# Optimization experiments

Hardware: AMD Instinct MI355X
Metric: run time of the kernel (lower is better)

## Reference

```python
import jax, jax.numpy as jnp
import numpy as np

N_NODES = 100000
N_EDGES = 3200000
N_GRAPHS = 128
F_IN, HID = 16, 64


def setup_inputs() -> dict:
    key = jax.random.key(0)
    ks = jax.random.split(key, 16)
    def lin(k, fan_in, fan_out):
        bound = 1.0 / np.sqrt(fan_in)
        kw, kb = jax.random.split(k)
        W = jax.random.uniform(kw, (fan_in, fan_out), jnp.float32, -bound, bound)
        b = jax.random.uniform(kb, (fan_out,), jnp.float32, -bound, bound)
        return W, b
    x = jax.random.normal(ks[0], (N_NODES, F_IN), jnp.float32)
    edge_index = jax.random.randint(ks[1], (2, N_EDGES), 0, N_NODES, jnp.int64 if jax.config.jax_enable_x64 else jnp.int32)
    edge_attr = jax.random.normal(ks[2], (N_EDGES, 4), jnp.float32)
    batch = jnp.sort(jax.random.randint(ks[3], (N_NODES,), 0, N_GRAPHS))
    W1, b1 = lin(ks[4], F_IN, HID)
    W2, b2 = lin(ks[5], HID, HID)
    W3, b3 = lin(ks[6], HID, HID)
    Wf1, bf1 = lin(ks[7], HID, 32)
    Wf2, bf2 = lin(ks[8], 32, 1)
    return dict(x=x, edge_index=edge_index, edge_attr=edge_attr, batch=batch,
                W1=W1, b1=b1, W2=W2, b2=b2, W3=W3, b3=b3,
                Wf1=Wf1, bf1=bf1, Wf2=Wf2, bf2=bf2)


def _gcn_conv(x, src, dst, norm, W, b, n_nodes):
    # PyG GCNConv: out = scatter_add(norm * (x @ W)[src] -> dst) + b
    h = x @ W                                   # [N, out]
    msg = h[src] * norm[:, None]                # [E+N, out] gather + scale
    agg = jax.ops.segment_sum(msg, dst, num_segments=n_nodes)
    return agg + b


def reference(x, edge_index, edge_attr, batch, W1, b1, W2, b2, W3, b3, Wf1, bf1, Wf2, bf2):
    n = x.shape[0]
    # add self loops (GCNConv default)
    loop = jnp.arange(n, dtype=edge_index.dtype)
    src = jnp.concatenate([edge_index[0], loop])
    dst = jnp.concatenate([edge_index[1], loop])
    # symmetric degree normalization: deg computed on dst with self loops
    deg = jax.ops.segment_sum(jnp.ones_like(src, dtype=x.dtype), dst, num_segments=n)
    dinv = jax.lax.rsqrt(jnp.maximum(deg, 1.0))
    norm = dinv[src] * dinv[dst]

    h = jax.nn.relu(_gcn_conv(x, src, dst, norm, W1, b1, n))   # dropout = identity (eval)
    h = jax.nn.relu(_gcn_conv(h, src, dst, norm, W2, b2, n))
    h = jax.nn.relu(_gcn_conv(h, src, dst, norm, W3, b3, n))

    # global mean pool over graphs
    sums = jax.ops.segment_sum(h, batch, num_segments=N_GRAPHS)          # [B, HID]
    cnts = jax.ops.segment_sum(jnp.ones((n,), x.dtype), batch, num_segments=N_GRAPHS)
    pooled = sums / jnp.maximum(cnts, 1.0)[:, None]

    z = jax.nn.relu(pooled @ Wf1 + bf1)
    return z @ Wf2 + bf2                                                  # [B, 1]
```

## Files before the change

### kernel.cpp

```cpp
#include <hip/hip_runtime.h>
#include <hip/hip_bf16.h>

#define HID 64
#define MAXNB 2048
#define NBLK 128
#define FILL_T 1024
#define SENT 0xFFFFFFFFu

__device__ __forceinline__ float bf2f(unsigned short u) {
    return __uint_as_float(((unsigned)u) << 16);
}
__device__ __forceinline__ unsigned short f2bf(float f) {
    __hip_bfloat16 b = __float2bfloat16(f);
    return *(unsigned short*)&b;
}
__device__ __host__ __forceinline__ int ceil16(int c) { return (c + 15) & ~15; }


__global__ __launch_bounds__(FILL_T) void radix_hist_kernel(
    const int* __restrict__ ei, int* __restrict__ H, int* __restrict__ bhist,
    int* __restrict__ bhist_pad, int E, int NB, int C) {
    __shared__ int lh[MAXNB];
    int blk = blockIdx.x, tid = threadIdx.x;
    for (int i = tid; i < NB; i += FILL_T) lh[i] = 0;
    __syncthreads();
    int lo = blk * C, hi = min(lo + C, E);
    for (int e = lo + tid; e < hi; e += FILL_T) atomicAdd(&lh[ei[E + e] >> 6], 1);
    __syncthreads();
    for (int i = tid; i < NB; i += FILL_T) {
        int v = lh[i];
        H[blk * NB + i] = v;
        if (v) {
            atomicAdd(&bhist[i], v);
            atomicAdd(&bhist_pad[i], ceil16(v));
        }
    }
}

__global__ __launch_bounds__(256) void scan_kernel(
    const int* __restrict__ bhist, const int* __restrict__ bhist_pad,
    int* __restrict__ pptr, int* __restrict__ cptr, int* __restrict__ gcur, int NB) {
    __shared__ int ssum[256];
    __shared__ int psum[256];
    int tid = threadIdx.x;
    int C = (NB + 255) / 256;
    int lo = tid * C, hi = min(lo + C, NB);
    int s = 0, p = 0;
    for (int i = lo; i < hi; i++) { s += bhist[i]; p += bhist_pad[i]; }
    ssum[tid] = s; psum[tid] = p;
    __syncthreads();
    for (int off = 1; off < 256; off <<= 1) {
        int v = (tid >= off) ? ssum[tid - off] : 0;
        int w = (tid >= off) ? psum[tid - off] : 0;
        __syncthreads();
        ssum[tid] += v; psum[tid] += w;
        __syncthreads();
    }
    int runc = (tid == 0) ? 0 : ssum[tid - 1];
    int runp = (tid == 0) ? 0 : psum[tid - 1];
    for (int i = lo; i < hi; i++) {
        cptr[i] = runc;
        pptr[i] = runp;
        gcur[i] = runp;
        runc += bhist[i];
        runp += bhist_pad[i];
    }
    if (hi == NB) { cptr[NB] = runc; pptr[NB] = runp; }
}

__global__ __launch_bounds__(FILL_T) void radix_fill_kernel(
    const int* __restrict__ ei, const int* __restrict__ H, int* __restrict__ gcur,
    unsigned* __restrict__ ebuf, int E, int NB, int C) {
    __shared__ int lcur[MAXNB];
    __shared__ int lend[MAXNB];
    int blk = blockIdx.x, tid = threadIdx.x;
    for (int i = tid; i < NB; i += FILL_T) {
        int cntb = H[blk * NB + i];
        int padc = ceil16(cntb);
        int start = padc ? atomicAdd(&gcur[i], padc) : 0;
        lcur[i] = start;
        lend[i] = start + padc;
    }
    __syncthreads();
    int lo = blk * C, hi = min(lo + C, E);
    for (int e = lo + tid; e < hi; e += FILL_T) {
        int s = ei[e];
        int d = ei[E + e];
        int pos = atomicAdd(&lcur[d >> 6], 1);
        ebuf[pos] = ((unsigned)s << 6) | (unsigned)(d & 63);
    }
    __syncthreads();
    for (int i = tid; i < NB; i += FILL_T) {
        for (int p = lcur[i]; p < lend[i]; p++) ebuf[p] = SENT;
    }
}

__global__ __launch_bounds__(256) void node_csr_kernel(
    const int* __restrict__ pptr, const int* __restrict__ cptr,
    const unsigned* __restrict__ ebuf,
    int* __restrict__ row_ptr, int* __restrict__ col, float* __restrict__ dinv,
    int N, int NB) {
    __shared__ int lcnt[64];
    __shared__ int loff[64];
    __shared__ int lcur[64];
    int bkt = blockIdx.x, tid = threadIdx.x;
    int beg = pptr[bkt], end = pptr[bkt + 1];
    int cbeg = cptr[bkt];
    if (tid < 64) lcnt[tid] = 0;
    __syncthreads();
    for (int e = beg + tid; e < end; e += 256) {
        unsigned ev = ebuf[e];
        if (ev != SENT) atomicAdd(&lcnt[ev & 63u], 1);
    }
    __syncthreads();
    if (tid == 0) {
        int run = cbeg;
        for (int i = 0; i < 64; i++) { loff[i] = run; lcur[i] = run; run += lcnt[i]; }
    }
    __syncthreads();
    if (tid < 64) {
        int node = (bkt << 6) + tid;
        if (node < N) {
            row_ptr[node] = loff[tid];
            dinv[node] = rsqrtf((float)(lcnt[tid] + 1));
        }
    }
    if (tid == 0 && bkt == NB - 1) row_ptr[N] = cptr[NB];
    for (int e = beg + tid; e < end; e += 256) {
        unsigned ev = ebuf[e];
        if (ev == SENT) continue;
        int pos = atomicAdd(&lcur[ev & 63u], 1);
        col[pos] = (int)(ev >> 6);
    }
}

template <typename Tin, int K>
__global__ void gemm_g_kernel(const Tin* __restrict__ in,
                              const float* __restrict__ W,
                              const float* __restrict__ dinv,
                              unsigned short* __restrict__ g, int N) {
    __shared__ float sW[K * HID];
    __shared__ float sIn[16 * K];
    int tid = threadIdx.x;
    for (int idx = tid; idx < K * HID; idx += 256) sW[idx] = W[idx];
    int base = blockIdx.x * 16;
    for (int idx = tid; idx < 16 * K; idx += 256) {
        int r = idx / K, c = idx % K;
        int node = base + r;
        float v = 0.f;
        if (node < N) {
            Tin t = in[(long long)node * K + c];
            if constexpr (sizeof(Tin) == 2) v = bf2f((unsigned short)t);
            else v = (float)t;
        }
        sIn[idx] = v;
    }
    __syncthreads();
    int j = tid & 63;
    int si = tid >> 6;
#pragma unroll
    for (int u = 0; u < 4; u++) {
        int r = si * 4 + u;
        int node = base + r;
        if (node >= N) continue;
        float acc = 0.f;
#pragma unroll
        for (int k = 0; k < K; k++) acc += sIn[r * K + k] * sW[k * HID + j];
        g[(long long)node * HID + j] = f2bf(dinv[node] * acc);
    }
}

__global__ __launch_bounds__(256) void gather_kernel(
    const int* __restrict__ row_ptr, const int* __restrict__ col,
    const unsigned short* __restrict__ g, const float* __restrict__ dinv,
    const float* __restrict__ bias, unsigned short* __restrict__ h, int N) {
    int wv = __builtin_amdgcn_readfirstlane(threadIdx.x >> 6);
    int node = blockIdx.x * 4 + wv;
    int lane = threadIdx.x & 63;
    if (node >= N) return;
    int beg = row_ptr[node], end = row_ptr[node + 1];
    float sum = bf2f(g[(long long)node * HID + lane]);
    int j = beg;
    for (; j + 8 <= end; j += 8) {
        int s0 = col[j + 0], s1 = col[j + 1], s2 = col[j + 2], s3 = col[j + 3];
        int s4 = col[j + 4], s5 = col[j + 5], s6 = col[j + 6], s7 = col[j + 7];
        float f0 = bf2f(g[(long long)s0 * HID + lane]);
        float f1 = bf2f(g[(long long)s1 * HID + lane]);
        float f2 = bf2f(g[(long long)s2 * HID + lane]);
        float f3 = bf2f(g[(long long)s3 * HID + lane]);
        float f4 = bf2f(g[(long long)s4 * HID + lane]);
        float f5 = bf2f(g[(long long)s5 * HID + lane]);
        float f6 = bf2f(g[(long long)s6 * HID + lane]);
        float f7 = bf2f(g[(long long)s7 * HID + lane]);
        sum += ((f0 + f1) + (f2 + f3)) + ((f4 + f5) + (f6 + f7));
    }
    for (; j < end; j++) {
        sum += bf2f(g[(long long)col[j] * HID + lane]);
    }
    float v = dinv[node] * sum + bias[lane];
    h[(long long)node * HID + lane] = f2bf(v > 0.f ? v : 0.f);
}

__global__ void pool_kernel(const unsigned short* __restrict__ h, const int* __restrict__ batch,
                            float* __restrict__ sums, float* __restrict__ cnt, int N) {
    int wave = blockIdx.x * 4 + (threadIdx.x >> 6);
    int lane = threadIdx.x & 63;
    int lo = wave * 64;
    if (lo >= N) return;
    int hi = min(lo + 64, N);
    int curb = batch[lo];
    float sum = 0.f;
    int nseg = 0;
    for (int i = lo; i < hi; i++) {
        int b = batch[i];
        if (b != curb) {
            atomicAdd(&sums[curb * HID + lane], sum);
            if (lane == 0) atomicAdd(&cnt[curb], (float)nseg);
            curb = b; sum = 0.f; nseg = 0;
        }
        sum += bf2f(h[(long long)i * HID + lane]);
        nseg++;
    }
    atomicAdd(&sums[curb * HID + lane], sum);
    if (lane == 0) atomicAdd(&cnt[curb], (float)nseg);
}

__global__ void final_kernel(const float* __restrict__ sums, const float* __restrict__ cnt,
                             const float* __restrict__ Wf1, const float* __restrict__ bf1,
                             const float* __restrict__ Wf2, const float* __restrict__ bf2,
                             float* __restrict__ out) {
    __shared__ float sW1[HID * 32];
    __shared__ float sW2[32];
    int tid = threadIdx.x;
    for (int idx = tid; idx < HID * 32; idx += 128) sW1[idx] = Wf1[idx];
    if (tid < 32) sW2[tid] = Wf2[tid];
    __syncthreads();
    int b = tid;
    float pooled[HID];
    float c = fmaxf(cnt[b], 1.0f);
#pragma unroll
    for (int j = 0; j < HID; j++) pooled[j] = sums[b * HID + j] / c;
    float o = bf2[0];
#pragma unroll 4
    for (int hd = 0; hd < 32; hd++) {
        float z = bf1[hd];
#pragma unroll
        for (int j = 0; j < HID; j++) z += pooled[j] * sW1[j * 32 + hd];
        z = fmaxf(z, 0.f);
        o += z * sW2[hd];
    }
    out[b] = o;
}

extern "C" void kernel_launch(void* const* d_in, const int* in_sizes, int n_in,
                              void* d_out, int out_size, void* d_ws, size_t ws_size,
                              hipStream_t stream) {
    const float* x     = (const float*)d_in[0];
    const int*   ei    = (const int*)d_in[1];
    const int*   batch = (const int*)d_in[3];
    const float* W1  = (const float*)d_in[4];
    const float* b1  = (const float*)d_in[5];
    const float* W2  = (const float*)d_in[6];
    const float* b2  = (const float*)d_in[7];
    const float* W3  = (const float*)d_in[8];
    const float* b3  = (const float*)d_in[9];
    const float* Wf1 = (const float*)d_in[10];
    const float* bf1 = (const float*)d_in[11];
    const float* Wf2 = (const float*)d_in[12];
    const float* bf2 = (const float*)d_in[13];
    float* out = (float*)d_out;

    const int N  = in_sizes[0] / 16;
    const int E  = in_sizes[1] / 2;
    const int NB = (N + 63) / 64;
    const size_t EBUF_CAP = (size_t)E + (size_t)NBLK * NB * 15;

    char* ws = (char*)d_ws;
    size_t o = 0;
    float*          dinv    = (float*)(ws + o);          o += ((size_t)N * 4 + 4095) / 4096 * 4096;
    int*            row_ptr = (int*)(ws + o);            o += ((size_t)(N + 1) * 4 + 4095) / 4096 * 4096;
    int*            pptr    = (int*)(ws + o);            o += ((size_t)(NB + 1) * 4 + 4095) / 4096 * 4096;
    int*            cptr    = (int*)(ws + o);            o += ((size_t)(NB + 1) * 4 + 4095) / 4096 * 4096;
    int*            bhist   = (int*)(ws + o);            o += ((size_t)(2 * NB) * 4 + 4095) / 4096 * 4096;
    int*            bhist_pad = bhist + NB;
    int*            gcur    = (int*)(ws + o);            o += ((size_t)NB * 4 + 4095) / 4096 * 4096;
    int*            H       = (int*)(ws + o);            o += ((size_t)NBLK * NB * 4 + 4095) / 4096 * 4096;
    unsigned*       ebuf    = (unsigned*)(ws + o);       o += EBUF_CAP * 4;
    int*            col     = (int*)(ws + o);            o += (size_t)E * 4;
    unsigned short* A       = (unsigned short*)(ws + o); o += (size_t)N * HID * 2;
    unsigned short* B       = (unsigned short*)(ws + o); o += (size_t)N * HID * 2;
    float*          sums    = (float*)(ws + o);          o += 128 * HID * 4;
    float*          cnt     = (float*)(ws + o);          o += 128 * 4;
    (void)ws_size;

    const int T = 256;
    const int Cchunk = (E + NBLK - 1) / NBLK;
    const int gGm = (N + 15) / 16;
    const int gGa = (N + 3) / 4;
    const int gPool = ((N + 63) / 64 + 3) / 4;

    hipMemsetAsync(bhist, 0, (size_t)(2 * NB) * 4, stream);
    radix_hist_kernel<<<NBLK, FILL_T, 0, stream>>>(ei, H, bhist, bhist_pad, E, NB, Cchunk);
    scan_kernel<<<1, T, 0, stream>>>(bhist, bhist_pad, pptr, cptr, gcur, NB);
    radix_fill_kernel<<<NBLK, FILL_T, 0, stream>>>(ei, H, gcur, ebuf, E, NB, Cchunk);
    node_csr_kernel<<<NB, T, 0, stream>>>(pptr, cptr, ebuf, row_ptr, col, dinv, N, NB);

    gemm_g_kernel<float, 16><<<gGm, T, 0, stream>>>(x, W1, dinv, A, N);
    gather_kernel<<<gGa, T, 0, stream>>>(row_ptr, col, A, dinv, b1, B, N);

    gemm_g_kernel<unsigned short, 64><<<gGm, T, 0, stream>>>(B, W2, dinv, B, N);
    gather_kernel<<<gGa, T, 0, stream>>>(row_ptr, col, B, dinv, b2, A, N);

    gemm_g_kernel<unsigned short, 64><<<gGm, T, 0, stream>>>(A, W3, dinv, A, N);
    gather_kernel<<<gGa, T, 0, stream>>>(row_ptr, col, A, dinv, b3, B, N);

    hipMemsetAsync(sums, 0, (128 * HID + 128) * 4, stream);
    pool_kernel<<<gPool, T, 0, stream>>>(B, batch, sums, cnt, N);
    final_kernel<<<1, 128, 0, stream>>>(sums, cnt, Wf1, bf1, Wf2, bf2, out);
}
```

Baseline: 574.8 us.

## Drop padded radix buckets, replicate shared histograms, vectorize edge loads

Removes the 16-aligned padding and sentinel fill from the radix bucketing, so the edge buffer is dense and the CSR build no longer skips sentinels or needs a separate padded scan. The histogram kernel uses four replicated shared-memory histograms to reduce atomic contention. Histogram and fill kernels read edges as int4 vectors, and the block count goes from 128 to 512. The per-bucket node scan now uses a wave shuffle, and the pool kernel gives each wave fewer nodes. Without padding, bucket segments written by different blocks may no longer start on aligned boundaries, which can make the scattered writes less coalesced.

```diff
diff --git a/kernel.cpp b/kernel.cpp
--- a/kernel.cpp
+++ b/kernel.cpp
@@ -3,9 +3,9 @@
 
 #define HID 64
 #define MAXNB 2048
-#define NBLK 128
+#define NBLK 512
 #define FILL_T 1024
-#define SENT 0xFFFFFFFFu
+#define HREP 4
 
 __device__ __forceinline__ float bf2f(unsigned short u) {
     return __uint_as_float(((unsigned)u) << 16);
@@ -14,90 +14,101 @@
     __hip_bfloat16 b = __float2bfloat16(f);
     return *(unsigned short*)&b;
 }
-__device__ __host__ __forceinline__ int ceil16(int c) { return (c + 15) & ~15; }
 
 
 __global__ __launch_bounds__(FILL_T) void radix_hist_kernel(
     const int* __restrict__ ei, int* __restrict__ H, int* __restrict__ bhist,
-    int* __restrict__ bhist_pad, int E, int NB, int C) {
-    __shared__ int lh[MAXNB];
+    int E, int NB, int C) {
+    __shared__ int lh[HREP * (MAXNB + 1)];
     int blk = blockIdx.x, tid = threadIdx.x;
-    for (int i = tid; i < NB; i += FILL_T) lh[i] = 0;
-    __syncthreads();
+    for (int i = tid; i < HREP * (MAXNB + 1); i += FILL_T) lh[i] = 0;
+    __syncthreads();
+    int* lhr = lh + ((tid >> 6) & (HREP - 1)) * (MAXNB + 1);
     int lo = blk * C, hi = min(lo + C, E);
-    for (int e = lo + tid; e < hi; e += FILL_T) atomicAdd(&lh[ei[E + e] >> 6], 1);
+    int cnt = hi - lo;
+    int n4 = ((E & 3) == 0) ? (cnt >> 2) : 0;
+    const int4* d4 = (const int4*)(ei + (long long)E + lo);
+    for (int k = tid; k < n4; k += FILL_T) {
+        int4 d = d4[k];
+        atomicAdd(&lhr[d.x >> 6], 1);
+        atomicAdd(&lhr[d.y >> 6], 1);
+        atomicAdd(&lhr[d.z >> 6], 1);
+        atomicAdd(&lhr[d.w >> 6], 1);
+    }
+    for (int e = lo + (n4 << 2) + tid; e < hi; e += FILL_T)
+        atomicAdd(&lhr[ei[(long long)E + e] >> 6], 1);
     __syncthreads();
     for (int i = tid; i < NB; i += FILL_T) {
-        int v = lh[i];
+        int v = 0;
+#pragma unroll
+        for (int r = 0; r < HREP; r++) v += lh[r * (MAXNB + 1) + i];
         H[blk * NB + i] = v;
-        if (v) {
-            atomicAdd(&bhist[i], v);
-            atomicAdd(&bhist_pad[i], ceil16(v));
-        }
+        if (v) atomicAdd(&bhist[i], v);
     }
 }
 
 __global__ __launch_bounds__(256) void scan_kernel(
-    const int* __restrict__ bhist, const int* __restrict__ bhist_pad,
-    int* __restrict__ pptr, int* __restrict__ cptr, int* __restrict__ gcur, int NB) {
+    const int* __restrict__ bhist, int* __restrict__ pptr, int* __restrict__ gcur, int NB) {
     __shared__ int ssum[256];
-    __shared__ int psum[256];
     int tid = threadIdx.x;
     int C = (NB + 255) / 256;
     int lo = tid * C, hi = min(lo + C, NB);
-    int s = 0, p = 0;
-    for (int i = lo; i < hi; i++) { s += bhist[i]; p += bhist_pad[i]; }
-    ssum[tid] = s; psum[tid] = p;
+    int s = 0;
+    for (int i = lo; i < hi; i++) s += bhist[i];
+    ssum[tid] = s;
     __syncthreads();
     for (int off = 1; off < 256; off <<= 1) {
         int v = (tid >= off) ? ssum[tid - off] : 0;
-        int w = (tid >= off) ? psum[tid - off] : 0;
         __syncthreads();
-        ssum[tid] += v; psum[tid] += w;
+        ssum[tid] += v;
         __syncthreads();
     }
-    int runc = (tid == 0) ? 0 : ssum[tid - 1];
-    int runp = (tid == 0) ? 0 : psum[tid - 1];
+    int run = (tid == 0) ? 0 : ssum[tid - 1];
     for (int i = lo; i < hi; i++) {
-        cptr[i] = runc;
-        pptr[i] = runp;
-        gcur[i] = runp;
-        runc += bhist[i];
-        runp += bhist_pad[i];
-    }
-    if (hi == NB) { cptr[NB] = runc; pptr[NB] = runp; }
+        pptr[i] = run;
+        gcur[i] = run;
+        run += bhist[i];
+    }
+    if (hi == NB) pptr[NB] = run;
 }
 
 __global__ __launch_bounds__(FILL_T) void radix_fill_kernel(
     const int* __restrict__ ei, const int* __restrict__ H, int* __restrict__ gcur,
     unsigned* __restrict__ ebuf, int E, int NB, int C) {
     __shared__ int lcur[MAXNB];
-    __shared__ int lend[MAXNB];
     int blk = blockIdx.x, tid = threadIdx.x;
     for (int i = tid; i < NB; i += FILL_T) {
-        int cntb = H[blk * NB + i];
-        int padc = ceil16(cntb);
-        int start = padc ? atomicAdd(&gcur[i], padc) : 0;
-        lcur[i] = start;
-        lend[i] = start + padc;
+        int c = H[blk * NB + i];
+        lcur[i] = c ? atomicAdd(&gcur[i], c) : 0;
     }
     __syncthreads();
     int lo = blk * C, hi = min(lo + C, E);
-    for (int e = lo + tid; e < hi; e += FILL_T) {
+    int cnt = hi - lo;
+    int n4 = ((E & 3) == 0) ? (cnt >> 2) : 0;
+    const int4* s4 = (const int4*)(ei + lo);
+    const int4* d4 = (const int4*)(ei + (long long)E + lo);
+    for (int k = tid; k < n4; k += FILL_T) {
+        int4 s = s4[k];
+        int4 d = d4[k];
+        int p0 = atomicAdd(&lcur[d.x >> 6], 1);
+        int p1 = atomicAdd(&lcur[d.y >> 6], 1);
+        int p2 = atomicAdd(&lcur[d.z >> 6], 1);
+        int p3 = atomicAdd(&lcur[d.w >> 6], 1);
+        ebuf[p0] = ((unsigned)s.x << 6) | (unsigned)(d.x & 63);
+        ebuf[p1] = ((unsigned)s.y << 6) | (unsigned)(d.y & 63);
+        ebuf[p2] = ((unsigned)s.z << 6) | (unsigned)(d.z & 63);
+        ebuf[p3] = ((unsigned)s.w << 6) | (unsigned)(d.w & 63);
+    }
+    for (int e = lo + (n4 << 2) + tid; e < hi; e += FILL_T) {
         int s = ei[e];
-        int d = ei[E + e];
+        int d = ei[(long long)E + e];
         int pos = atomicAdd(&lcur[d >> 6], 1);
         ebuf[pos] = ((unsigned)s << 6) | (unsigned)(d & 63);
     }
-    __syncthreads();
-    for (int i = tid; i < NB; i += FILL_T) {
-        for (int p = lcur[i]; p < lend[i]; p++) ebuf[p] = SENT;
-    }
 }
 
 __global__ __launch_bounds__(256) void node_csr_kernel(
-    const int* __restrict__ pptr, const int* __restrict__ cptr,
-    const unsigned* __restrict__ ebuf,
+    const int* __restrict__ pptr, const unsigned* __restrict__ ebuf,
     int* __restrict__ row_ptr, int* __restrict__ col, float* __restrict__ dinv,
     int N, int NB) {
     __shared__ int lcnt[64];
@@ -105,30 +116,31 @@
     __shared__ int lcur[64];
     int bkt = blockIdx.x, tid = threadIdx.x;
     int beg = pptr[bkt], end = pptr[bkt + 1];
-    int cbeg = cptr[bkt];
     if (tid < 64) lcnt[tid] = 0;
+    __syncthreads();
+    for (int e = beg + tid; e < end; e += 256) atomicAdd(&lcnt[ebuf[e] & 63u], 1);
+    __syncthreads();
+    if (tid < 64) {
+        int v = lcnt[tid];
+        int p = v;
+#pragma unroll
+        for (int off = 1; off < 64; off <<= 1) {
+            int t = __shfl_up(p, off);
+            if (tid >= off) p += t;
+        }
+        int base = beg + p - v;
+        loff[tid] = base;
+        lcur[tid] = base;
+        int node = (bkt << 6) + tid;
+        if (node < N) {
+            row_ptr[node] = base;
+            dinv[node] = rsqrtf((float)(v + 1));
+        }
+    }
+    if (tid == 0 && bkt == NB - 1) row_ptr[N] = pptr[NB];
     __syncthreads();
     for (int e = beg + tid; e < end; e += 256) {
         unsigned ev = ebuf[e];
-        if (ev != SENT) atomicAdd(&lcnt[ev & 63u], 1);
-    }
-    __syncthreads();
-    if (tid == 0) {
-        int run = cbeg;
-        for (int i = 0; i < 64; i++) { loff[i] = run; lcur[i] = run; run += lcnt[i]; }
-    }
-    __syncthreads();
-    if (tid < 64) {
-        int node = (bkt << 6) + tid;
-        if (node < N) {
-            row_ptr[node] = loff[tid];
-            dinv[node] = rsqrtf((float)(lcnt[tid] + 1));
-        }
-    }
-    if (tid == 0 && bkt == NB - 1) row_ptr[N] = cptr[NB];
-    for (int e = beg + tid; e < end; e += 256) {
-        unsigned ev = ebuf[e];
-        if (ev == SENT) continue;
         int pos = atomicAdd(&lcur[ev & 63u], 1);
         col[pos] = (int)(ev >> 6);
     }
@@ -205,9 +217,9 @@
                             float* __restrict__ sums, float* __restrict__ cnt, int N) {
     int wave = blockIdx.x * 4 + (threadIdx.x >> 6);
     int lane = threadIdx.x & 63;
-    int lo = wave * 64;
+    int lo = wave * 16;
     if (lo >= N) return;
-    int hi = min(lo + 64, N);
+    int hi = min(lo + 16, N);
     int curb = batch[lo];
     float sum = 0.f;
     int nseg = 0;
@@ -273,19 +285,16 @@
     const int N  = in_sizes[0] / 16;
     const int E  = in_sizes[1] / 2;
     const int NB = (N + 63) / 64;
-    const size_t EBUF_CAP = (size_t)E + (size_t)NBLK * NB * 15;
 
     char* ws = (char*)d_ws;
     size_t o = 0;
     float*          dinv    = (float*)(ws + o);          o += ((size_t)N * 4 + 4095) / 4096 * 4096;
     int*            row_ptr = (int*)(ws + o);            o += ((size_t)(N + 1) * 4 + 4095) / 4096 * 4096;
     int*            pptr    = (int*)(ws + o);            o += ((size_t)(NB + 1) * 4 + 4095) / 4096 * 4096;
-    int*            cptr    = (int*)(ws + o);            o += ((size_t)(NB + 1) * 4 + 4095) / 4096 * 4096;
-    int*            bhist   = (int*)(ws + o);            o += ((size_t)(2 * NB) * 4 + 4095) / 4096 * 4096;
-    int*            bhist_pad = bhist + NB;
+    int*            bhist   = (int*)(ws + o);            o += ((size_t)NB * 4 + 4095) / 4096 * 4096;
     int*            gcur    = (int*)(ws + o);            o += ((size_t)NB * 4 + 4095) / 4096 * 4096;
     int*            H       = (int*)(ws + o);            o += ((size_t)NBLK * NB * 4 + 4095) / 4096 * 4096;
-    unsigned*       ebuf    = (unsigned*)(ws + o);       o += EBUF_CAP * 4;
+    unsigned*       ebuf    = (unsigned*)(ws + o);       o += (size_t)E * 4;
     int*            col     = (int*)(ws + o);            o += (size_t)E * 4;
     unsigned short* A       = (unsigned short*)(ws + o); o += (size_t)N * HID * 2;
     unsigned short* B       = (unsigned short*)(ws + o); o += (size_t)N * HID * 2;
@@ -294,16 +303,16 @@
     (void)ws_size;
 
     const int T = 256;
-    const int Cchunk = (E + NBLK - 1) / NBLK;
+    const int Cchunk = (((E + NBLK - 1) / NBLK) + 3) & ~3;
     const int gGm = (N + 15) / 16;
     const int gGa = (N + 3) / 4;
-    const int gPool = ((N + 63) / 64 + 3) / 4;
-
-    hipMemsetAsync(bhist, 0, (size_t)(2 * NB) * 4, stream);
-    radix_hist_kernel<<<NBLK, FILL_T, 0, stream>>>(ei, H, bhist, bhist_pad, E, NB, Cchunk);
-    scan_kernel<<<1, T, 0, stream>>>(bhist, bhist_pad, pptr, cptr, gcur, NB);
+    const int gPool = ((N + 15) / 16 + 3) / 4;
+
+    hipMemsetAsync(bhist, 0, (size_t)NB * 4, stream);
+    radix_hist_kernel<<<NBLK, FILL_T, 0, stream>>>(ei, H, bhist, E, NB, Cchunk);
+    scan_kernel<<<1, T, 0, stream>>>(bhist, pptr, gcur, NB);
     radix_fill_kernel<<<NBLK, FILL_T, 0, stream>>>(ei, H, gcur, ebuf, E, NB, Cchunk);
-    node_csr_kernel<<<NB, T, 0, stream>>>(pptr, cptr, ebuf, row_ptr, col, dinv, N, NB);
+    node_csr_kernel<<<NB, T, 0, stream>>>(pptr, ebuf, row_ptr, col, dinv, N, NB);
 
     gemm_g_kernel<float, 16><<<gGm, T, 0, stream>>>(x, W1, dinv, A, N);
     gather_kernel<<<gGa, T, 0, stream>>>(row_ptr, col, A, dinv, b1, B, N);
```

Result: faster. 549.4 us (-4.4%).
